# Performance work log

Hardware: AMD Instinct MI355X
Metric: run time of the kernel (lower is better)

## Reference

```python
import jax, jax.numpy as jnp
import numpy as np


def setup_inputs() -> dict:
    key = jax.random.key(0)
    k1, k2 = jax.random.split(key)
    N, C, H, W = 8, 256, 96, 96
    Cw, KK = 32, 9  # groups=8 -> C_w = C/8; ks=3 -> K*K=9
    x = jax.random.normal(k1, (N, C, H, W), dtype=jnp.float32)
    w = jax.random.normal(k2, (N, Cw, KK, H, W), dtype=jnp.float32)
    return {"x": x, "w": w}


def reference(x, w):
    # x: (N, C, H, W); w: (N, C_w, K*K, H, W)
    N, C, H, W = x.shape
    Cw, KK = w.shape[1], w.shape[2]
    K = int(np.sqrt(KK))
    pad = (K - 1) // 2
    G = C // Cw
    xp = jnp.pad(x, ((0, 0), (0, 0), (pad, pad), (pad, pad)))
    out = jnp.zeros((N, G, Cw, H, W), dtype=x.dtype)
    # accumulate over the K*K taps without materializing the full window tensor;
    # window index k = a*K + b corresponds to xp[..., h+a, w+b]
    for k in range(KK):
        a, b = divmod(k, K)
        win = xp[:, :, a:a + H, b:b + W].reshape(N, G, Cw, H, W)
        out = out + win * w[:, None, :, k]
    return out.reshape(N, C, H, W)
```

## Files before the change

kernel.cpp:

```cpp
#include <hip/hip_runtime.h>
#include <stdint.h>


#define N_  8
#define C_  256
#define H_  96
#define W_  96
#define CW_ 32
#define G_  8
#define PL_ (H_ * W_)

typedef float f32x4 __attribute__((ext_vector_type(4)));

__global__ __launch_bounds__(64, 4) void SKA_kernel(const float* __restrict__ x,
                                                    const float* __restrict__ wgt,
                                                    float* __restrict__ out) {
    __shared__ float xs[4 * G_ * W_];

    const int lane  = threadIdx.x;
    const int widx  = lane & 31;
    const int rowid = lane >> 5;

    const int b  = blockIdx.x;
    const int lb = (b & 7) * 1536 + (b >> 3);
    const int ht = lb % 48;
    const int t1 = lb / 48;
    const int cw = t1 % CW_;
    const int n  = t1 / CW_;
    const int h0 = ht * 2;
    const int h  = h0 + rowid;
    const int w0a = widx * 4;
    const int w0  = (w0a > W_ - 4) ? (W_ - 4) : w0a;
    const bool active = (widx < 24);

    const float* wb = wgt + (size_t)(((n * CW_ + cw) * 9) * H_ + h) * W_ + w0;
    f32x4 wv[9];
#pragma unroll
    for (int k = 0; k < 9; ++k)
        wv[k] = __builtin_nontemporal_load(reinterpret_cast<const f32x4*>(wb + k * PL_));

    const int nc = (n * C_ + cw) * PL_;
    int goff[3], csel[3];
#pragma unroll
    for (int cc = 0; cc < 3; ++cc) {
        const int wo = cc * 256 + lane * 4;
        goff[cc] = (wo / 96) * (CW_ * PL_);
        csel[cc] = wo % 96;
    }
#pragma unroll
    for (int r = 0; r < 4; ++r) {
        int row = h0 - 1 + r;
        row = row < 0 ? 0 : (row > H_ - 1 ? H_ - 1 : row);
#pragma unroll
        for (int cc = 0; cc < 3; ++cc) {
            const int off = nc + goff[cc] + row * W_ + csel[cc];
            const uint32_t lds_off = (uint32_t)(uintptr_t)&xs[(r * 3 + cc) * 256];
            __builtin_amdgcn_global_load_lds(
                (const __attribute__((address_space(1))) void*)(uintptr_t)(x + off),
                (__attribute__((address_space(3))) void*)lds_off,
                16, 0, 0);
        }
    }

    __builtin_amdgcn_sched_barrier(0);
    asm volatile("s_waitcnt vmcnt(0)" ::: "memory");
    __builtin_amdgcn_sched_barrier(0);

    f32x4 acc[G_];
#pragma unroll
    for (int g = 0; g < G_; ++g) acc[g] = (f32x4)(0.f);

#pragma unroll
    for (int a = 0; a < 3; ++a) {
        const int hh = h + a - 1;
        if (hh < 0 || hh >= H_) continue;
        const f32x4 wa = wv[a * 3 + 0];
        const f32x4 wm = wv[a * 3 + 1];
        const f32x4 wc = wv[a * 3 + 2];
#pragma unroll
        for (int g = 0; g < G_; ++g) {
            const f32x4 xm = *reinterpret_cast<const f32x4*>(
                &xs[(rowid + a) * (G_ * W_) + g * W_ + w0]);
            float xl = __shfl(xm.w, lane - 1);
            float xr = __shfl(xm.x, lane + 1);
            xl = (widx == 0) ? 0.f : xl;
            xr = (widx == 23) ? 0.f : xr;
            acc[g].x = fmaf(xl,   wa.x, acc[g].x);
            acc[g].x = fmaf(xm.x, wm.x, acc[g].x);
            acc[g].x = fmaf(xm.y, wc.x, acc[g].x);
            acc[g].y = fmaf(xm.x, wa.y, acc[g].y);
            acc[g].y = fmaf(xm.y, wm.y, acc[g].y);
            acc[g].y = fmaf(xm.z, wc.y, acc[g].y);
            acc[g].z = fmaf(xm.y, wa.z, acc[g].z);
            acc[g].z = fmaf(xm.z, wm.z, acc[g].z);
            acc[g].z = fmaf(xm.w, wc.z, acc[g].z);
            acc[g].w = fmaf(xm.z, wa.w, acc[g].w);
            acc[g].w = fmaf(xm.w, wm.w, acc[g].w);
            acc[g].w = fmaf(xr,   wc.w, acc[g].w);
        }
    }

    if (active) {
        float* ob = out + nc + h * W_ + w0a;
#pragma unroll
        for (int g = 0; g < G_; ++g)
            __builtin_nontemporal_store(acc[g],
                reinterpret_cast<f32x4*>(ob + g * (CW_ * PL_)));
    }
}

extern "C" void kernel_launch(void* const* d_in, const int* in_sizes, int n_in,
                              void* d_out, int out_size, void* d_ws, size_t ws_size,
                              hipStream_t stream) {
    const float* x   = (const float*)d_in[0];
    const float* wgt = (const float*)d_in[1];
    float* out = (float*)d_out;

    constexpr int grid = N_ * CW_ * (H_ / 2);
    SKA_kernel<<<grid, 64, 0, stream>>>(x, wgt, out);
}
```

Baseline: 43.91 us.

## Make blocks persistent over row tiles with double-buffered async LDS staging

Each block now covers 16 rows (8 tiles of 2 rows) instead of one 2-row tile, so the grid shrinks from 12288 to 1536 blocks. Both x rows and weights are staged into double-buffered LDS with global_load_lds, and the next tile is prefetched while the current one computes, gated by partial vmcnt waits. The aim is to hide load latency and cut per-block launch overhead. The cost is fewer blocks, which may underfill the GPU, and waitcnt accounting that depends on stores also being counted by vmcnt.

New measurement: 50.13 us. 1.14x slower.

```diff
diff --git a/kernel.cpp b/kernel.cpp
--- a/kernel.cpp
+++ b/kernel.cpp
@@ -9,103 +9,144 @@
 #define CW_ 32
 #define G_  8
 #define PL_ (H_ * W_)
+#define TILES_ 8
+#define XFL_ 3072
+#define WFL_ 1792
 
 typedef float f32x4 __attribute__((ext_vector_type(4)));
 
-__global__ __launch_bounds__(64, 4) void SKA_kernel(const float* __restrict__ x,
-                                                    const float* __restrict__ wgt,
-                                                    float* __restrict__ out) {
-    __shared__ float xs[4 * G_ * W_];
+__global__ __launch_bounds__(64) void SKA_kernel(const float* __restrict__ x,
+                                                 const float* __restrict__ wgt,
+                                                 float* __restrict__ out) {
+    __shared__ float xs[2 * XFL_ + 2 * WFL_];
 
     const int lane  = threadIdx.x;
     const int widx  = lane & 31;
     const int rowid = lane >> 5;
 
-    const int b  = blockIdx.x;
-    const int lb = (b & 7) * 1536 + (b >> 3);
-    const int ht = lb % 48;
-    const int t1 = lb / 48;
-    const int cw = t1 % CW_;
-    const int n  = t1 / CW_;
-    const int h0 = ht * 2;
-    const int h  = h0 + rowid;
+    const int b    = blockIdx.x;
+    const int lb   = (b & 7) * 192 + (b >> 3);
+    const int hcol = lb % 6;
+    const int cw   = (lb / 6) % CW_;
+    const int n    = lb / 192;
+
+    const int nc  = (n * C_ + cw) * PL_;
+    const int wk0 = (n * CW_ + cw) * 9;
+
     const int w0a = widx * 4;
     const int w0  = (w0a > W_ - 4) ? (W_ - 4) : w0a;
     const bool active = (widx < 24);
 
-    const float* wb = wgt + (size_t)(((n * CW_ + cw) * 9) * H_ + h) * W_ + w0;
-    f32x4 wv[9];
-#pragma unroll
-    for (int k = 0; k < 9; ++k)
-        wv[k] = __builtin_nontemporal_load(reinterpret_cast<const f32x4*>(wb + k * PL_));
-
-    const int nc = (n * C_ + cw) * PL_;
-    int goff[3], csel[3];
+    int xgoff[3], xcol[3];
 #pragma unroll
     for (int cc = 0; cc < 3; ++cc) {
         const int wo = cc * 256 + lane * 4;
-        goff[cc] = (wo / 96) * (CW_ * PL_);
-        csel[cc] = wo % 96;
+        xgoff[cc] = (wo / 96) * (CW_ * PL_);
+        xcol[cc]  = wo % 96;
     }
+    int wkoff[7], wroff[7], wcol[7];
 #pragma unroll
-    for (int r = 0; r < 4; ++r) {
-        int row = h0 - 1 + r;
-        row = row < 0 ? 0 : (row > H_ - 1 ? H_ - 1 : row);
+    for (int cc = 0; cc < 7; ++cc) {
+        int e = cc * 256 + lane * 4;
+        if (e > 1724) e = 1724;
+        wkoff[cc] = e / 192;
+        wroff[cc] = (e % 192) / 96;
+        wcol[cc]  = e % 96;
+    }
+
+    auto stage = [&](int buf, int t) {
+        const int h0t = hcol * 16 + 2 * t;
+        const uint32_t xb = (uint32_t)(buf * XFL_);
 #pragma unroll
-        for (int cc = 0; cc < 3; ++cc) {
-            const int off = nc + goff[cc] + row * W_ + csel[cc];
-            const uint32_t lds_off = (uint32_t)(uintptr_t)&xs[(r * 3 + cc) * 256];
+        for (int r = 0; r < 4; ++r) {
+            int row = h0t - 1 + r;
+            row = row < 0 ? 0 : (row > H_ - 1 ? H_ - 1 : row);
+#pragma unroll
+            for (int cc = 0; cc < 3; ++cc) {
+                const int off = nc + xgoff[cc] + row * W_ + xcol[cc];
+                __builtin_amdgcn_global_load_lds(
+                    (const __attribute__((address_space(1))) void*)(uintptr_t)(x + off),
+                    (__attribute__((address_space(3))) void*)(uintptr_t)
+                        (uint32_t)(uintptr_t)&xs[xb + (r * 3 + cc) * 256],
+                    16, 0, 0);
+            }
+        }
+        const uint32_t wb2 = (uint32_t)(2 * XFL_ + buf * WFL_);
+#pragma unroll
+        for (int cc = 0; cc < 7; ++cc) {
+            const int off = ((wk0 + wkoff[cc]) * H_ + h0t + wroff[cc]) * W_ + wcol[cc];
             __builtin_amdgcn_global_load_lds(
-                (const __attribute__((address_space(1))) void*)(uintptr_t)(x + off),
-                (__attribute__((address_space(3))) void*)lds_off,
+                (const __attribute__((address_space(1))) void*)(uintptr_t)(wgt + off),
+                (__attribute__((address_space(3))) void*)(uintptr_t)
+                    (uint32_t)(uintptr_t)&xs[wb2 + cc * 256],
                 16, 0, 0);
         }
-    }
+    };
 
-    __builtin_amdgcn_sched_barrier(0);
-    asm volatile("s_waitcnt vmcnt(0)" ::: "memory");
-    __builtin_amdgcn_sched_barrier(0);
+    stage(0, 0);
 
-    f32x4 acc[G_];
+#pragma unroll 1
+    for (int t = 0; t < TILES_; ++t) {
+        const int cur = t & 1;
+        if (t + 1 < TILES_) stage(cur ^ 1, t + 1);
+        __builtin_amdgcn_sched_barrier(0);
+        if (t + 1 < TILES_) {
+            asm volatile("s_waitcnt vmcnt(19)" ::: "memory");
+        } else {
+            asm volatile("s_waitcnt vmcnt(8)" ::: "memory");
+        }
+        __builtin_amdgcn_sched_barrier(0);
+
+        const int h   = hcol * 16 + 2 * t + rowid;
+        const float* xbuf = &xs[cur * XFL_];
+        const float* wbuf = &xs[2 * XFL_ + cur * WFL_];
+
+        f32x4 wv[9];
 #pragma unroll
-    for (int g = 0; g < G_; ++g) acc[g] = (f32x4)(0.f);
+        for (int k = 0; k < 9; ++k)
+            wv[k] = *reinterpret_cast<const f32x4*>(&wbuf[k * 192 + rowid * 96 + w0]);
+
+        f32x4 acc[G_];
+#pragma unroll
+        for (int g = 0; g < G_; ++g) acc[g] = (f32x4)(0.f);
 
 #pragma unroll
-    for (int a = 0; a < 3; ++a) {
-        const int hh = h + a - 1;
-        if (hh < 0 || hh >= H_) continue;
-        const f32x4 wa = wv[a * 3 + 0];
-        const f32x4 wm = wv[a * 3 + 1];
-        const f32x4 wc = wv[a * 3 + 2];
+        for (int a = 0; a < 3; ++a) {
+            const int hh = h + a - 1;
+            if (hh < 0 || hh >= H_) continue;
+            const f32x4 wa = wv[a * 3 + 0];
+            const f32x4 wm = wv[a * 3 + 1];
+            const f32x4 wc = wv[a * 3 + 2];
 #pragma unroll
-        for (int g = 0; g < G_; ++g) {
-            const f32x4 xm = *reinterpret_cast<const f32x4*>(
-                &xs[(rowid + a) * (G_ * W_) + g * W_ + w0]);
-            float xl = __shfl(xm.w, lane - 1);
-            float xr = __shfl(xm.x, lane + 1);
-            xl = (widx == 0) ? 0.f : xl;
-            xr = (widx == 23) ? 0.f : xr;
-            acc[g].x = fmaf(xl,   wa.x, acc[g].x);
-            acc[g].x = fmaf(xm.x, wm.x, acc[g].x);
-            acc[g].x = fmaf(xm.y, wc.x, acc[g].x);
-            acc[g].y = fmaf(xm.x, wa.y, acc[g].y);
-            acc[g].y = fmaf(xm.y, wm.y, acc[g].y);
-            acc[g].y = fmaf(xm.z, wc.y, acc[g].y);
-            acc[g].z = fmaf(xm.y, wa.z, acc[g].z);
-            acc[g].z = fmaf(xm.z, wm.z, acc[g].z);
-            acc[g].z = fmaf(xm.w, wc.z, acc[g].z);
-            acc[g].w = fmaf(xm.z, wa.w, acc[g].w);
-            acc[g].w = fmaf(xm.w, wm.w, acc[g].w);
-            acc[g].w = fmaf(xr,   wc.w, acc[g].w);
+            for (int g = 0; g < G_; ++g) {
+                const f32x4 xm = *reinterpret_cast<const f32x4*>(
+                    &xbuf[(rowid + a) * (G_ * W_) + g * W_ + w0]);
+                float xl = __shfl(xm.w, lane - 1);
+                float xr = __shfl(xm.x, lane + 1);
+                xl = (widx == 0) ? 0.f : xl;
+                xr = (widx == 23) ? 0.f : xr;
+                acc[g].x = fmaf(xl,   wa.x, acc[g].x);
+                acc[g].x = fmaf(xm.x, wm.x, acc[g].x);
+                acc[g].x = fmaf(xm.y, wc.x, acc[g].x);
+                acc[g].y = fmaf(xm.x, wa.y, acc[g].y);
+                acc[g].y = fmaf(xm.y, wm.y, acc[g].y);
+                acc[g].y = fmaf(xm.z, wc.y, acc[g].y);
+                acc[g].z = fmaf(xm.y, wa.z, acc[g].z);
+                acc[g].z = fmaf(xm.z, wm.z, acc[g].z);
+                acc[g].z = fmaf(xm.w, wc.z, acc[g].z);
+                acc[g].w = fmaf(xm.z, wa.w, acc[g].w);
+                acc[g].w = fmaf(xm.w, wm.w, acc[g].w);
+                acc[g].w = fmaf(xr,   wc.w, acc[g].w);
+            }
         }
-    }
 
-    if (active) {
-        float* ob = out + nc + h * W_ + w0a;
+        if (active) {
+            float* ob = out + nc + h * W_ + w0a;
 #pragma unroll
-        for (int g = 0; g < G_; ++g)
-            __builtin_nontemporal_store(acc[g],
-                reinterpret_cast<f32x4*>(ob + g * (CW_ * PL_)));
+            for (int g = 0; g < G_; ++g)
+                __builtin_nontemporal_store(acc[g],
+                    reinterpret_cast<f32x4*>(ob + g * (CW_ * PL_)));
+        }
     }
 }
 
@@ -116,6 +157,6 @@
     const float* wgt = (const float*)d_in[1];
     float* out = (float*)d_out;
 
-    constexpr int grid = N_ * CW_ * (H_ / 2);
+    constexpr int grid = N_ * CW_ * 6;
     SKA_kernel<<<grid, 64, 0, stream>>>(x, wgt, out);
 }
```
